# Kernel tuning notes

Measured on AMD Instinct MI355X. Metric: run time of the kernel, lower is better.

## Reference

```python
import jax, jax.numpy as jnp
import numpy as np

N_EMBD = 1024
N_HEAD = 16
HEAD_DIM = N_EMBD // N_HEAD
EPS = 1e-5


def setup_inputs() -> dict:
    key = jax.random.key(0)
    ks = jax.random.split(key, 12)
    C = N_EMBD
    s = lambda fan_in: 1.0 / np.sqrt(fan_in)
    return {
        "x": jax.random.normal(ks[0], (2, 2048, C), dtype=jnp.float32),
        "ln1_g": jnp.ones((C,), jnp.float32),
        "ln1_b": jnp.zeros((C,), jnp.float32),
        "w_attn": jax.random.normal(ks[1], (C, 3 * C), jnp.float32) * s(C),
        "b_attn": jnp.zeros((3 * C,), jnp.float32),
        "w_proj": jax.random.normal(ks[2], (C, C), jnp.float32) * s(C),
        "b_proj": jnp.zeros((C,), jnp.float32),
        "ln2_g": jnp.ones((C,), jnp.float32),
        "ln2_b": jnp.zeros((C,), jnp.float32),
        "w_fc": jax.random.normal(ks[3], (C, 4 * C), jnp.float32) * s(C),
        "b_fc": jnp.zeros((4 * C,), jnp.float32),
        "w_fc2": jax.random.normal(ks[4], (4 * C, C), jnp.float32) * s(4 * C),
        "b_fc2": jnp.zeros((C,), jnp.float32),
    }


def _layernorm(x, g, b):
    mu = jnp.mean(x, axis=-1, keepdims=True)
    var = jnp.mean(jnp.square(x - mu), axis=-1, keepdims=True)
    return (x - mu) * jax.lax.rsqrt(var + EPS) * g + b


def _attention(x, w_attn, b_attn, w_proj, b_proj):
    B, T, C = x.shape
    qkv = x @ w_attn + b_attn  # [B,T,3C]
    q, k, v = jnp.split(qkv, 3, axis=-1)
    # [B,H,T,D]
    reshape = lambda t: t.reshape(B, T, N_HEAD, HEAD_DIM).transpose(0, 2, 1, 3)
    q, k, v = reshape(q), reshape(k), reshape(v)
    scale = HEAD_DIM ** (-0.5)
    att = jnp.einsum("bhqd,bhkd->bhqk", q, k) * scale  # [B,H,T,T]
    mask = jnp.tril(jnp.ones((T, T), dtype=bool))
    att = jnp.where(mask, att, -jnp.inf)
    att = jax.nn.softmax(att, axis=-1)
    y = jnp.einsum("bhqk,bhkd->bhqd", att, v)
    y = y.transpose(0, 2, 1, 3).reshape(B, T, C)
    return y @ w_proj + b_proj


def _mlp(x, w_fc, b_fc, w_fc2, b_fc2):
    h = jax.nn.gelu(x @ w_fc + b_fc, approximate=False)  # nn.GELU default = exact erf
    return h @ w_fc2 + b_fc2


def reference(x, ln1_g, ln1_b, w_attn, b_attn, w_proj, b_proj,
              ln2_g, ln2_b, w_fc, b_fc, w_fc2, b_fc2):
    x = x + _attention(_layernorm(x, ln1_g, ln1_b), w_attn, b_attn, w_proj, b_proj)
    x = x + _mlp(_layernorm(x, ln2_g, ln2_b), w_fc, b_fc, w_fc2, b_fc2)
    return x
```

## Files before the change

kernel.cpp:

```cpp
#include <hip/hip_runtime.h>
#include <hip/hip_bf16.h>
#include <math.h>

typedef __attribute__((ext_vector_type(8))) __bf16 bf16x8;
typedef __attribute__((ext_vector_type(4))) float floatx4;
typedef __attribute__((ext_vector_type(8))) unsigned short ushort8;

#define C_EMBD 1024
#define T_SEQ 2048
#define NH 16
#define HD 64

#define WAITV(N) asm volatile("s_waitcnt vmcnt(" #N ")" ::: "memory")
#define WAITL(N) asm volatile("s_waitcnt lgkmcnt(" #N ")" ::: "memory")
#define DSR(d, a, OFF) \
  asm volatile("ds_read_b128 %0, %1 offset:" #OFF : "=v"(d) : "v"(a))

static __device__ __forceinline__ unsigned short f2b(float f) {
  __hip_bfloat16 h = __float2bfloat16(f);
  unsigned short u;
  __builtin_memcpy(&u, &h, sizeof(u));
  return u;
}
static __device__ __forceinline__ float b2f(unsigned short u) {
  unsigned int b = ((unsigned int)u) << 16;
  float f;
  __builtin_memcpy(&f, &b, sizeof(f));
  return f;
}

static __device__ __forceinline__ void gload16(const void* g, void* l) {
  __builtin_amdgcn_global_load_lds(
      (__attribute__((address_space(1))) void*)(void*)g,
      (__attribute__((address_space(3))) void*)l, 16, 0, 0);
}

static __device__ __forceinline__ floatx4 mfma_bf16(bf16x8 a, bf16x8 b, floatx4 c) {
  return __builtin_amdgcn_mfma_f32_16x16x32_bf16(a, b, c, 0, 0, 0);
}

static __device__ __forceinline__ unsigned int lds_addr(const void* p) {
  return (unsigned int)(size_t)(__attribute__((address_space(3))) void*)(void*)p;
}

__global__ __launch_bounds__(256) void wtrans(const float* __restrict__ in,
                                              unsigned short* __restrict__ out,
                                              int K, int N) {
  __shared__ float t[32][33];
  int n0 = blockIdx.x * 32, k0 = blockIdx.y * 32;
  int tx = threadIdx.x & 31, ty = threadIdx.x >> 5;
#pragma unroll
  for (int i = 0; i < 4; i++)
    t[ty + i * 8][tx] = in[(size_t)(k0 + ty + i * 8) * N + n0 + tx];
  __syncthreads();
#pragma unroll
  for (int i = 0; i < 4; i++)
    out[(size_t)(n0 + ty + i * 8) * K + k0 + tx] = f2b(t[tx][ty + i * 8]);
}

__global__ __launch_bounds__(256) void ln_fwd(const float* __restrict__ x,
                                              const float* __restrict__ g,
                                              const float* __restrict__ bta,
                                              unsigned short* __restrict__ out) {
  int row = blockIdx.x;
  int t = threadIdx.x;
  const float4* xr = (const float4*)(x + (size_t)row * C_EMBD);
  float4 v = xr[t];
  float s = v.x + v.y + v.z + v.w;
  float ss = v.x * v.x + v.y * v.y + v.z * v.z + v.w * v.w;
#pragma unroll
  for (int m = 1; m < 64; m <<= 1) {
    s += __shfl_xor(s, m, 64);
    ss += __shfl_xor(ss, m, 64);
  }
  __shared__ float ps[8];
  int wv = t >> 6;
  if ((t & 63) == 0) { ps[wv] = s; ps[4 + wv] = ss; }
  __syncthreads();
  s = ps[0] + ps[1] + ps[2] + ps[3];
  ss = ps[4] + ps[5] + ps[6] + ps[7];
  float mu = s * (1.0f / C_EMBD);
  float var = ss * (1.0f / C_EMBD) - mu * mu;
  float rs = rsqrtf(var + 1e-5f);
  float4 gv = ((const float4*)g)[t];
  float4 bv = ((const float4*)bta)[t];
  ushort4 o;
  o.x = f2b((v.x - mu) * rs * gv.x + bv.x);
  o.y = f2b((v.y - mu) * rs * gv.y + bv.y);
  o.z = f2b((v.z - mu) * rs * gv.z + bv.z);
  o.w = f2b((v.w - mu) * rs * gv.w + bv.w);
  *(ushort4*)(out + (size_t)row * C_EMBD + t * 4) = o;
}

template <int EP, int MI>
__global__ __launch_bounds__(256) void gemm_bt(const unsigned short* __restrict__ A,
                                               const unsigned short* __restrict__ Bt,
                                               const float* __restrict__ bias,
                                               const float* __restrict__ res,
                                               void* __restrict__ outv,
                                               unsigned short* __restrict__ vt,
                                               int M, int N, int K) {
  __shared__ __align__(16) unsigned short As[MI * 32 * 32];
  __shared__ __align__(16) unsigned short Bs[128 * 32];
  const int tid = threadIdx.x;
  const int wv = tid >> 6, ln = tid & 63;
  const int quad = ln >> 4, l15 = ln & 15;
  const int wm = wv >> 1, wn = wv & 1;
  const int m0 = blockIdx.y * (MI * 32), n0 = blockIdx.x * 128;

  floatx4 acc[MI][4];
#pragma unroll
  for (int i = 0; i < MI; i++)
#pragma unroll
    for (int j = 0; j < 4; j++) acc[i][j] = (floatx4)0.0f;

  const int rowA = ln >> 2;
  const int koff = (ln & 3) * 8;

  for (int k0 = 0; k0 < K; k0 += 32) {
    if (k0) __syncthreads();
#pragma unroll
    for (int hh = 0; hh < MI / 2; ++hh) {
      int r = hh * 64 + wv * 16 + rowA;
      gload16(A + (size_t)(m0 + r) * K + k0 + koff, &As[(hh * 64 + wv * 16) * 32]);
    }
#pragma unroll
    for (int hh = 0; hh < 2; ++hh) {
      int r = hh * 64 + wv * 16 + rowA;
      gload16(Bt + (size_t)(n0 + r) * K + k0 + koff, &Bs[(hh * 64 + wv * 16) * 32]);
    }
    __syncthreads();
    bf16x8 af[MI], bfr[4];
#pragma unroll
    for (int mi = 0; mi < MI; mi++)
      af[mi] = *(const bf16x8*)&As[(wm * (MI * 16) + mi * 16 + l15) * 32 + quad * 8];
#pragma unroll
    for (int ni = 0; ni < 4; ni++)
      bfr[ni] = *(const bf16x8*)&Bs[(wn * 64 + ni * 16 + l15) * 32 + quad * 8];
#pragma unroll
    for (int mi = 0; mi < MI; mi++)
#pragma unroll
      for (int ni = 0; ni < 4; ni++)
        acc[mi][ni] = mfma_bf16(af[mi], bfr[ni], acc[mi][ni]);
  }

#pragma unroll
  for (int mi = 0; mi < MI; mi++) {
#pragma unroll
    for (int ni = 0; ni < 4; ni++) {
      int col = n0 + wn * 64 + ni * 16 + l15;
      int rowb = m0 + wm * (MI * 16) + mi * 16 + quad * 4;
      float bc = bias[col];
      if (EP == 1) {
#pragma unroll
        for (int r = 0; r < 4; r++) {
          size_t idx = (size_t)(rowb + r) * N + col;
          ((float*)outv)[idx] = acc[mi][ni][r] + bc + res[idx];
        }
      }
    }
  }
}

#define MFROW(av, m)                               \
  acc[m][0] = mfma_bf16(av, bF0, acc[m][0]);       \
  acc[m][1] = mfma_bf16(av, bF1, acc[m][1]);       \
  acc[m][2] = mfma_bf16(av, bF2, acc[m][2]);       \
  acc[m][3] = mfma_bf16(av, bF3, acc[m][3]);

template <int EP>
__global__ __launch_bounds__(512, 2) void gemm256(
    const unsigned short* __restrict__ A, const unsigned short* __restrict__ Bt,
    const float* __restrict__ bias, const float* __restrict__ res,
    void* __restrict__ outv, unsigned short* __restrict__ vt,
    float* __restrict__ p0, float* __restrict__ p12,
    int M, int N, int ldK, int KCH) {
  __shared__ __align__(16) unsigned short As[4][8192];
  __shared__ __align__(16) unsigned short Bs[4][8192];
  const int tid = threadIdx.x;
  const int wv = tid >> 6, ln = tid & 63;
  const int quad = ln >> 4, l15 = ln & 15;
  const int wm = wv >> 2, wn = wv & 3;

  const int gx = gridDim.x;
  const int nwg = gx * gridDim.y;
  int id = blockIdx.y * gx + blockIdx.x;
  const int cpx = nwg >> 3;
  id = (id & 7) * cpx + (id >> 3);
  const int n0 = (id % gx) * 256;
  const int m0 = (id / gx) * 256;
  const int bz = blockIdx.z;

  A += (size_t)bz * KCH;
  Bt += (size_t)bz * KCH;

  const int srowin = ln >> 2;
  const int sqo = ((ln & 3) ^ (ln >> 4)) * 8;
  const unsigned short* aSt = A + (size_t)(m0 + wv * 16 + srowin) * ldK + sqo;
  const unsigned short* bSt = Bt + (size_t)(n0 + wv * 16 + srowin) * ldK + sqo;
  const size_t gstep = (size_t)128 * ldK;

  const int fswb = (quad ^ (l15 >> 2)) * 16;
  const unsigned int aoff =
      lds_addr(&As[0][0]) + (unsigned)((wm * 128 + l15) * 64 + fswb);
  const unsigned int boff =
      lds_addr(&Bs[0][0]) + (unsigned)((wn * 64 + l15) * 64 + fswb);

  floatx4 acc[8][4];
#pragma unroll
  for (int i = 0; i < 8; i++)
#pragma unroll
    for (int j = 0; j < 4; j++) acc[i][j] = (floatx4)0.0f;

  const int NT = KCH >> 5;

  auto stageh = [&](int bi, int kt, int g) {
    gload16(aSt + kt * 32 + (size_t)g * gstep, &As[bi][g * 4096 + wv * 512]);
    gload16(bSt + kt * 32 + (size_t)g * gstep, &Bs[bi][g * 4096 + wv * 512]);
  };

  stageh(0, 0, 0); stageh(0, 0, 1);
  stageh(1, 1, 0); stageh(1, 1, 1);
  stageh(2, 2, 0); stageh(2, 2, 1);

  for (int t = 0; t < NT; ++t) {
    const int cur = t & 3;
    const int rem = NT - 1 - t;
    if (rem >= 2) WAITV(8);
    else if (rem == 1) WAITV(4);
    else WAITV(0);
    __builtin_amdgcn_s_barrier();

    const unsigned int ab = aoff + (cur << 14);
    const unsigned int bb = boff + (cur << 14);
    bf16x8 bF0, bF1, bF2, bF3, aA0, aA1, aA2, aA3;
    DSR(bF0, bb, 0); DSR(bF1, bb, 1024); DSR(bF2, bb, 2048); DSR(bF3, bb, 3072);
    DSR(aA0, ab, 0); DSR(aA1, ab, 1024); DSR(aA2, ab, 2048); DSR(aA3, ab, 3072);
    if (t + 3 < NT) stageh((t + 3) & 3, t + 3, 0);
    __builtin_amdgcn_s_barrier();
    WAITL(0);
    __builtin_amdgcn_sched_barrier(0);
    __builtin_amdgcn_s_setprio(1);
    MFROW(aA0, 0) MFROW(aA1, 1) MFROW(aA2, 2) MFROW(aA3, 3)
    __builtin_amdgcn_s_setprio(0);
    __builtin_amdgcn_s_barrier();

    bf16x8 aB0, aB1, aB2, aB3;
    DSR(aB0, ab, 4096); DSR(aB1, ab, 5120); DSR(aB2, ab, 6144); DSR(aB3, ab, 7168);
    if (t + 3 < NT) stageh((t + 3) & 3, t + 3, 1);
    __builtin_amdgcn_s_barrier();
    WAITL(0);
    __builtin_amdgcn_sched_barrier(0);
    __builtin_amdgcn_s_setprio(1);
    MFROW(aB0, 4) MFROW(aB1, 5) MFROW(aB2, 6) MFROW(aB3, 7)
    __builtin_amdgcn_s_setprio(0);
  }

#pragma unroll
  for (int mi = 0; mi < 8; mi++) {
#pragma unroll
    for (int ni = 0; ni < 4; ni++) {
      const int col = n0 + wn * 64 + ni * 16 + l15;
      const int rowb = m0 + wm * 128 + mi * 16 + quad * 4;
      const float bc = bias ? bias[col] : 0.0f;
      if (EP == 1) {
#pragma unroll
        for (int r = 0; r < 4; r++) {
          size_t idx = (size_t)(rowb + r) * N + col;
          ((float*)outv)[idx] = acc[mi][ni][r] + bc + res[idx];
        }
      } else if (EP == 2) {
#pragma unroll
        for (int r = 0; r < 4; r++) {
          float v = acc[mi][ni][r] + bc;
          v = 0.5f * v * (1.0f + erff(v * 0.70710678118f));
          ((unsigned short*)outv)[(size_t)(rowb + r) * N + col] = f2b(v);
        }
      } else if (EP == 3) {
        if (col < 2048) {
#pragma unroll
          for (int r = 0; r < 4; r++)
            ((unsigned short*)outv)[(size_t)(rowb + r) * N + col] =
                f2b(acc[mi][ni][r] + bc);
        } else {
          int dall = col - 2048;
          int hh2 = dall >> 6, dd = dall & 63;
          int bq = rowb >> 11, t0 = rowb & 2047;
          __align__(8) unsigned short pk[4];
#pragma unroll
          for (int r = 0; r < 4; r++) pk[r] = f2b(acc[mi][ni][r] + bc);
          *(ushort4*)&vt[(size_t)((bq * NH + hh2) * HD + dd) * T_SEQ + t0] =
              *(const ushort4*)pk;
        }
      } else {
        if (bz == 3) {
#pragma unroll
          for (int r = 0; r < 4; r++) {
            size_t idx = (size_t)(rowb + r) * N + col;
            ((float*)outv)[idx] = acc[mi][ni][r] + bc + res[idx];
          }
        } else {
          const size_t MN = (size_t)M * N;
          float* pp = (bz == 0) ? p0 : p12 + (size_t)(bz - 1) * MN;
#pragma unroll
          for (int r = 0; r < 4; r++)
            pp[(size_t)(rowb + r) * N + col] = acc[mi][ni][r];
        }
      }
    }
  }
}

__global__ __launch_bounds__(256) void red3(const float* __restrict__ p0,
                                            const float* __restrict__ p12,
                                            float* __restrict__ out) {
  const size_t MN4 = (size_t)4096 * 1024 / 4;
  for (size_t i = (size_t)blockIdx.x * 256 + threadIdx.x; i < MN4;
       i += (size_t)gridDim.x * 256) {
    float4 a = ((const float4*)p0)[i];
    float4 b = ((const float4*)p12)[i];
    float4 c = ((const float4*)p12)[i + MN4];
    float4 o = ((float4*)out)[i];
    o.x += a.x + b.x + c.x;
    o.y += a.y + b.y + c.y;
    o.z += a.z + b.z + c.z;
    o.w += a.w + b.w + c.w;
    ((float4*)out)[i] = o;
  }
}

__global__ __launch_bounds__(256) void attn_fwd(const unsigned short* __restrict__ qkv,
                                                const unsigned short* __restrict__ vt,
                                                unsigned short* __restrict__ y) {
  __shared__ __align__(16) unsigned short Ks[3][64 * 64];
  __shared__ __align__(16) unsigned short Vs[3][64 * 64];
  __shared__ __align__(16) unsigned short Ps[4 * 16 * 72];
  const int tid = threadIdx.x;
  const int wv = tid >> 6, ln = tid & 63;
  const int quad = ln >> 4, l15 = ln & 15;
  const int pair = blockIdx.x, h = blockIdx.y, b = blockIdx.z;
  unsigned short* Pw = &Ps[wv * 16 * 72];

  const unsigned short* kbase = qkv + (size_t)b * T_SEQ * 3072 + 1024 + h * HD;
  const unsigned short* vbase = vt + (size_t)(b * NH + h) * HD * T_SEQ;

  int koffs[2], voffs[2], ldst[2];
#pragma unroll
  for (int g = 0; g < 2; g++) {
    int S = wv * 128 + g * 64 + ln;
    int r = S >> 3;
    int c = (S & 7) ^ (r & 7);
    koffs[g] = r * 3072 + c * 8;
    voffs[g] = r * T_SEQ + c * 8;
    ldst[g] = wv * 1024 + g * 512;
  }

  auto stage = [&](int kt, int slot) {
#pragma unroll
    for (int g = 0; g < 2; g++) {
      gload16(kbase + (size_t)(kt * 64) * 3072 + koffs[g], &Ks[slot][ldst[g]]);
      gload16(vbase + kt * 64 + voffs[g], &Vs[slot][ldst[g]]);
    }
  };

  for (int ph = 0; ph < 2; ++ph) {
    const int qt = ph ? (31 - pair) : pair;
    const unsigned short* qp =
        qkv + (size_t)(b * T_SEQ + qt * 64 + wv * 16 + l15) * 3072 + h * HD;
    bf16x8 qf[2];
#pragma unroll
    for (int kc = 0; kc < 2; kc++) {
      ushort8 u = *(const ushort8*)(qp + kc * 32 + quad * 8);
      union { ushort8 u; bf16x8 v; } cv;
#pragma unroll
      for (int j = 0; j < 8; j++) cv.u[j] = f2b(b2f(u[j]) * 0.18033688f);
      qf[kc] = cv.v;
    }

    floatx4 o[4];
#pragma unroll
    for (int dt = 0; dt < 4; dt++) o[dt] = (floatx4)0.0f;
    float lacc = 0.0f;

    stage(0, 0);
    if (qt >= 1) stage(1, 1);

    for (int kt = 0; kt <= qt; ++kt) {
      const int slot = kt % 3;
      const bool diag = (kt == qt);
      if (kt < qt) WAITV(4); else WAITV(0);
      __builtin_amdgcn_s_barrier();
      if (kt + 2 <= qt) stage(kt + 2, (kt + 2) % 3);

      const unsigned short* Kc = Ks[slot];
      const unsigned short* Vc = Vs[slot];
      floatx4 s[4];
#pragma unroll
      for (int nt = 0; nt < 4; nt++) s[nt] = (floatx4)0.0f;
#pragma unroll
      for (int nt = 0; nt < 4; nt++)
#pragma unroll
        for (int kc = 0; kc < 2; kc++) {
          bf16x8 kf = *(const bf16x8*)
              &Kc[(nt * 16 + l15) * 64 + (((kc * 4 + quad) ^ (l15 & 7)) * 8)];
          s[nt] = mfma_bf16(kf, qf[kc], s[nt]);
        }

      float psum = 0.0f;
#pragma unroll
      for (int nt = 0; nt < 4; nt++) {
        __align__(8) unsigned short pk[4];
#pragma unroll
        for (int r = 0; r < 4; r++) {
          float sv = s[nt][r];
          if (diag && (nt * 16 + quad * 4 + r > wv * 16 + l15)) sv = -1e30f;
          float p = exp2f(sv - 12.0f);
          psum += p;
          pk[r] = f2b(p);
        }
        *(ushort4*)&Pw[l15 * 72 + nt * 16 + quad * 4] = *(const ushort4*)pk;
      }
      lacc += psum;

      bf16x8 pf0 = *(const bf16x8*)&Pw[l15 * 72 + quad * 8];
      bf16x8 pf1 = *(const bf16x8*)&Pw[l15 * 72 + 32 + quad * 8];
#pragma unroll
      for (int dt = 0; dt < 4; dt++) {
        bf16x8 vf0 = *(const bf16x8*)
            &Vc[(dt * 16 + l15) * 64 + ((quad ^ (l15 & 7)) * 8)];
        bf16x8 vf1 = *(const bf16x8*)
            &Vc[(dt * 16 + l15) * 64 + (((4 + quad) ^ (l15 & 7)) * 8)];
        o[dt] = mfma_bf16(vf0, pf0, o[dt]);
        o[dt] = mfma_bf16(vf1, pf1, o[dt]);
      }
    }

    lacc += __shfl_xor(lacc, 16, 64);
    lacc += __shfl_xor(lacc, 32, 64);
    float rinv = 1.0f / lacc;
#pragma unroll
    for (int dt = 0; dt < 4; dt++) {
      __align__(8) unsigned short ov[4];
#pragma unroll
      for (int r = 0; r < 4; r++) ov[r] = f2b(o[dt][r] * rinv);
      *(ushort4*)&y[(size_t)(b * T_SEQ + qt * 64 + wv * 16 + l15) * C_EMBD +
                    h * HD + dt * 16 + quad * 4] = *(const ushort4*)ov;
    }
  }
}

extern "C" void kernel_launch(void* const* d_in, const int* in_sizes, int n_in,
                              void* d_out, int out_size, void* d_ws, size_t ws_size,
                              hipStream_t stream) {
  (void)in_sizes; (void)n_in; (void)out_size; (void)ws_size;
  const float* x      = (const float*)d_in[0];
  const float* ln1_g  = (const float*)d_in[1];
  const float* ln1_b  = (const float*)d_in[2];
  const float* w_attn = (const float*)d_in[3];
  const float* b_attn = (const float*)d_in[4];
  const float* w_proj = (const float*)d_in[5];
  const float* b_proj = (const float*)d_in[6];
  const float* ln2_g  = (const float*)d_in[7];
  const float* ln2_b  = (const float*)d_in[8];
  const float* w_fc   = (const float*)d_in[9];
  const float* b_fc   = (const float*)d_in[10];
  const float* w_fc2  = (const float*)d_in[11];
  const float* b_fc2  = (const float*)d_in[12];
  float* out = (float*)d_out;

  char* wsb = (char*)d_ws;
  char* ws = wsb;
  unsigned short* wat  = (unsigned short*)ws; ws += (size_t)3072 * 1024 * 2;
  unsigned short* wpt  = (unsigned short*)ws; ws += (size_t)1024 * 1024 * 2;
  unsigned short* wft  = (unsigned short*)ws; ws += (size_t)4096 * 1024 * 2;
  unsigned short* wf2t = (unsigned short*)ws; ws += (size_t)1024 * 4096 * 2;
  unsigned short* xn   = (unsigned short*)ws; ws += (size_t)4096 * 1024 * 2;
  unsigned short* qkv  = (unsigned short*)ws; ws += (size_t)4096 * 3072 * 2;
  unsigned short* yat  = (unsigned short*)ws; ws += (size_t)4096 * 1024 * 2;
  unsigned short* hbuf = (unsigned short*)ws; ws += (size_t)4096 * 4096 * 2;
  unsigned short* vt = hbuf;
  float* p0  = (float*)wsb;
  float* p12 = (float*)(wsb + (size_t)24 * 1024 * 1024);

  wtrans<<<dim3(3072 / 32, 1024 / 32), 256, 0, stream>>>(w_attn, wat, 1024, 3072);
  wtrans<<<dim3(1024 / 32, 1024 / 32), 256, 0, stream>>>(w_proj, wpt, 1024, 1024);
  wtrans<<<dim3(4096 / 32, 1024 / 32), 256, 0, stream>>>(w_fc, wft, 1024, 4096);
  wtrans<<<dim3(1024 / 32, 4096 / 32), 256, 0, stream>>>(w_fc2, wf2t, 4096, 1024);

  ln_fwd<<<4096, 256, 0, stream>>>(x, ln1_g, ln1_b, xn);
  gemm256<3><<<dim3(3072 / 256, 4096 / 256), 512, 0, stream>>>(
      xn, wat, b_attn, nullptr, qkv, vt, nullptr, nullptr, 4096, 3072, 1024, 1024);
  attn_fwd<<<dim3(16, NH, 2), 256, 0, stream>>>(qkv, vt, yat);
  gemm_bt<1, 2><<<dim3(8, 64), 256, 0, stream>>>(
      yat, wpt, b_proj, x, out, nullptr, 4096, 1024, 1024);
  ln_fwd<<<4096, 256, 0, stream>>>(out, ln2_g, ln2_b, xn);
  gemm256<2><<<dim3(4096 / 256, 4096 / 256), 512, 0, stream>>>(
      xn, wft, b_fc, nullptr, hbuf, nullptr, nullptr, nullptr, 4096, 4096, 1024, 1024);
  gemm256<4><<<dim3(1024 / 256, 4096 / 256, 4), 512, 0, stream>>>(
      hbuf, wf2t, b_fc2, out, out, nullptr, p0, p12, 4096, 1024, 4096, 1024);
  red3<<<2048, 256, 0, stream>>>(p0, p12, out);
}
```

Before: 389.4 us.

## Switch 256x256 GEMM to BK=64 double-buffered LDS pipeline

Reworks the main 256x256 GEMM mainloop from a 4-stage ring of K=32 tiles to two buffers of K=64 tiles. The global-to-LDS staging layout and XOR swizzle change to match 128-byte rows. Next-tile B and A loads are issued interleaved with the two MFMA halves, and per-half barriers are dropped. This halves the number of loop iterations and barriers per K, at the cost of shallower prefetch depth. It also risks an LDS race, since A for the next tile is written into the other buffer without an intervening barrier.

```diff
diff --git a/kernel.cpp b/kernel.cpp
--- a/kernel.cpp
+++ b/kernel.cpp
@@ -162,12 +162,6 @@
   }
 }
 
-#define MFROW(av, m)                               \
-  acc[m][0] = mfma_bf16(av, bF0, acc[m][0]);       \
-  acc[m][1] = mfma_bf16(av, bF1, acc[m][1]);       \
-  acc[m][2] = mfma_bf16(av, bF2, acc[m][2]);       \
-  acc[m][3] = mfma_bf16(av, bF3, acc[m][3]);
-
 template <int EP>
 __global__ __launch_bounds__(512, 2) void gemm256(
     const unsigned short* __restrict__ A, const unsigned short* __restrict__ Bt,
@@ -175,8 +169,8 @@
     void* __restrict__ outv, unsigned short* __restrict__ vt,
     float* __restrict__ p0, float* __restrict__ p12,
     int M, int N, int ldK, int KCH) {
-  __shared__ __align__(16) unsigned short As[4][8192];
-  __shared__ __align__(16) unsigned short Bs[4][8192];
+  __shared__ __align__(16) unsigned short As[2][16384];
+  __shared__ __align__(16) unsigned short Bs[2][16384];
   const int tid = threadIdx.x;
   const int wv = tid >> 6, ln = tid & 63;
   const int quad = ln >> 4, l15 = ln & 15;
@@ -194,17 +188,18 @@
   A += (size_t)bz * KCH;
   Bt += (size_t)bz * KCH;
 
-  const int srowin = ln >> 2;
-  const int sqo = ((ln & 3) ^ (ln >> 4)) * 8;
-  const unsigned short* aSt = A + (size_t)(m0 + wv * 16 + srowin) * ldK + sqo;
-  const unsigned short* bSt = Bt + (size_t)(n0 + wv * 16 + srowin) * ldK + sqo;
-  const size_t gstep = (size_t)128 * ldK;
-
-  const int fswb = (quad ^ (l15 >> 2)) * 16;
-  const unsigned int aoff =
-      lds_addr(&As[0][0]) + (unsigned)((wm * 128 + l15) * 64 + fswb);
-  const unsigned int boff =
-      lds_addr(&Bs[0][0]) + (unsigned)((wn * 64 + l15) * 64 + fswb);
+  const unsigned short* aSt =
+      A + (size_t)(m0 + wv * 8 + (ln >> 3)) * ldK + (((ln & 7) ^ (ln >> 3)) * 8);
+  const unsigned short* bSt =
+      Bt + (size_t)(n0 + wv * 8 + (ln >> 3)) * ldK + (((ln & 7) ^ (ln >> 3)) * 8);
+  const size_t gstep = (size_t)64 * ldK;
+
+  const int sw0 = ((quad) ^ (l15 & 7)) * 16;
+  const int sw1 = ((4 + quad) ^ (l15 & 7)) * 16;
+  const unsigned int aoff0 = lds_addr(&As[0][0]) + (wm * 128 + l15) * 128 + sw0;
+  const unsigned int aoff1 = lds_addr(&As[0][0]) + (wm * 128 + l15) * 128 + sw1;
+  const unsigned int boff0 = lds_addr(&Bs[0][0]) + (wn * 64 + l15) * 128 + sw0;
+  const unsigned int boff1 = lds_addr(&Bs[0][0]) + (wn * 64 + l15) * 128 + sw1;
 
   floatx4 acc[8][4];
 #pragma unroll
@@ -212,47 +207,72 @@
 #pragma unroll
     for (int j = 0; j < 4; j++) acc[i][j] = (floatx4)0.0f;
 
-  const int NT = KCH >> 5;
-
-  auto stageh = [&](int bi, int kt, int g) {
-    gload16(aSt + kt * 32 + (size_t)g * gstep, &As[bi][g * 4096 + wv * 512]);
-    gload16(bSt + kt * 32 + (size_t)g * gstep, &Bs[bi][g * 4096 + wv * 512]);
+  const int NT = KCH >> 6;
+
+  auto stA1 = [&](int bi, int kt, int g) {
+    gload16(aSt + (size_t)kt * 64 + (size_t)g * gstep,
+            &As[bi][(g * 64 + wv * 8) * 64]);
   };
-
-  stageh(0, 0, 0); stageh(0, 0, 1);
-  stageh(1, 1, 0); stageh(1, 1, 1);
-  stageh(2, 2, 0); stageh(2, 2, 1);
+  auto stB1 = [&](int bi, int kt, int g) {
+    gload16(bSt + (size_t)kt * 64 + (size_t)g * gstep,
+            &Bs[bi][(g * 64 + wv * 8) * 64]);
+  };
+
+  stB1(0, 0, 0); stB1(0, 0, 1); stB1(0, 0, 2); stB1(0, 0, 3);
+  stA1(0, 0, 0); stA1(0, 0, 2); stA1(0, 0, 1); stA1(0, 0, 3);
 
   for (int t = 0; t < NT; ++t) {
-    const int cur = t & 3;
-    const int rem = NT - 1 - t;
-    if (rem >= 2) WAITV(8);
-    else if (rem == 1) WAITV(4);
-    else WAITV(0);
+    const int cur = t & 1;
+    const bool more = (t + 1 < NT);
+    WAITV(2);
     __builtin_amdgcn_s_barrier();
 
-    const unsigned int ab = aoff + (cur << 14);
-    const unsigned int bb = boff + (cur << 14);
-    bf16x8 bF0, bF1, bF2, bF3, aA0, aA1, aA2, aA3;
-    DSR(bF0, bb, 0); DSR(bF1, bb, 1024); DSR(bF2, bb, 2048); DSR(bF3, bb, 3072);
-    DSR(aA0, ab, 0); DSR(aA1, ab, 1024); DSR(aA2, ab, 2048); DSR(aA3, ab, 3072);
-    if (t + 3 < NT) stageh((t + 3) & 3, t + 3, 0);
-    __builtin_amdgcn_s_barrier();
+    const unsigned int ab0 = aoff0 + (cur << 15), ab1 = aoff1 + (cur << 15);
+    const unsigned int bb0 = boff0 + (cur << 15), bb1 = boff1 + (cur << 15);
+    bf16x8 bf0[4], bf1[4], af0[4], af1[4];
+    DSR(bf0[0], bb0, 0);    DSR(bf0[1], bb0, 2048);
+    DSR(bf0[2], bb0, 4096); DSR(bf0[3], bb0, 6144);
+    DSR(bf1[0], bb1, 0);    DSR(bf1[1], bb1, 2048);
+    DSR(bf1[2], bb1, 4096); DSR(bf1[3], bb1, 6144);
+    DSR(af0[0], ab0, 0);    DSR(af0[1], ab0, 2048);
+    DSR(af0[2], ab0, 4096); DSR(af0[3], ab0, 6144);
+    DSR(af1[0], ab1, 0);    DSR(af1[1], ab1, 2048);
+    DSR(af1[2], ab1, 4096); DSR(af1[3], ab1, 6144);
+    if (more) {
+      stB1(cur ^ 1, t + 1, 0); stB1(cur ^ 1, t + 1, 1);
+      stB1(cur ^ 1, t + 1, 2); stB1(cur ^ 1, t + 1, 3);
+    }
     WAITL(0);
     __builtin_amdgcn_sched_barrier(0);
     __builtin_amdgcn_s_setprio(1);
-    MFROW(aA0, 0) MFROW(aA1, 1) MFROW(aA2, 2) MFROW(aA3, 3)
+#pragma unroll
+    for (int mi = 0; mi < 4; mi++)
+#pragma unroll
+      for (int ni = 0; ni < 4; ni++) {
+        acc[mi][ni] = mfma_bf16(af0[mi], bf0[ni], acc[mi][ni]);
+        acc[mi][ni] = mfma_bf16(af1[mi], bf1[ni], acc[mi][ni]);
+      }
     __builtin_amdgcn_s_setprio(0);
-    __builtin_amdgcn_s_barrier();
-
-    bf16x8 aB0, aB1, aB2, aB3;
-    DSR(aB0, ab, 4096); DSR(aB1, ab, 5120); DSR(aB2, ab, 6144); DSR(aB3, ab, 7168);
-    if (t + 3 < NT) stageh((t + 3) & 3, t + 3, 1);
-    __builtin_amdgcn_s_barrier();
+
+    if (more) WAITV(4); else WAITV(0);
+    DSR(af0[0], ab0, 8192);  DSR(af0[1], ab0, 10240);
+    DSR(af0[2], ab0, 12288); DSR(af0[3], ab0, 14336);
+    DSR(af1[0], ab1, 8192);  DSR(af1[1], ab1, 10240);
+    DSR(af1[2], ab1, 12288); DSR(af1[3], ab1, 14336);
+    if (more) {
+      stA1(cur ^ 1, t + 1, 0); stA1(cur ^ 1, t + 1, 2);
+      stA1(cur ^ 1, t + 1, 1); stA1(cur ^ 1, t + 1, 3);
+    }
     WAITL(0);
     __builtin_amdgcn_sched_barrier(0);
     __builtin_amdgcn_s_setprio(1);
-    MFROW(aB0, 4) MFROW(aB1, 5) MFROW(aB2, 6) MFROW(aB3, 7)
+#pragma unroll
+    for (int mi = 0; mi < 4; mi++)
+#pragma unroll
+      for (int ni = 0; ni < 4; ni++) {
+        acc[4 + mi][ni] = mfma_bf16(af0[mi], bf0[ni], acc[4 + mi][ni]);
+        acc[4 + mi][ni] = mfma_bf16(af1[mi], bf1[ni], acc[4 + mi][ni]);
+      }
     __builtin_amdgcn_s_setprio(0);
   }
 
```

Measured after the change: 368.8 us. 5.3% less time.
